# Optimization experiments

Measured on AMD Instinct MI355X. Metric: run time of the kernel, lower is better.

Reference implementation:

```python
import jax, jax.numpy as jnp
import numpy as np

MAX_WAVELENGTH = 10000.0
NUM_HEADS = 15
NUM_KV_HEADS = 5
HEAD_DIM = 64


def apply_rope(x, positions):
    """RoPE: x [B, L, H, D], positions [B, L] (int)."""
    d_half = x.shape[-1] // 2
    x = x.astype(jnp.float32)
    freq_exponents = (2.0 / x.shape[-1]) * jnp.arange(d_half, dtype=jnp.float32)
    timescale = MAX_WAVELENGTH ** freq_exponents  # [d_half]
    radians = positions[..., None].astype(jnp.float32) / timescale  # [B, L, d_half]
    radians = radians[..., None, :]  # [B, L, 1, d_half]
    sin, cos = jnp.sin(radians), jnp.cos(radians)
    x1, x2 = x[..., :d_half], x[..., d_half:]
    return jnp.concatenate([x1 * cos - x2 * sin, x2 * cos + x1 * sin], axis=-1)


def setup_inputs() -> dict:
    key = jax.random.key(0)
    k1, k2, k3, k4 = jax.random.split(key, 4)
    B, L = 2, 2048
    query_states = jax.random.normal(k1, (B, L, NUM_HEADS, HEAD_DIM), dtype=jnp.float32)
    key_states = jax.random.normal(k2, (B, L, NUM_KV_HEADS, HEAD_DIM), dtype=jnp.float32)
    value_states = jax.random.normal(k3, (B, L, NUM_KV_HEADS, HEAD_DIM), dtype=jnp.float32)
    positions = jnp.sort(jax.random.randint(k4, (B, L), 0, L, dtype=jnp.int32), axis=-1)
    # Causal (prefix-LM) boolean mask [B, L, L]
    attention_mask = jnp.broadcast_to(jnp.tril(jnp.ones((L, L), dtype=bool)), (B, L, L))
    return {
        "query_states": query_states,
        "key_states": key_states,
        "value_states": value_states,
        "positions": positions,
        "attention_mask": attention_mask,
    }


def reference(query_states, key_states, value_states, positions, attention_mask):
    B, L = query_states.shape[0], query_states.shape[1]
    groups = NUM_HEADS // NUM_KV_HEADS  # 3

    # RoPE on Q and K (eager, per original module)
    q = apply_rope(query_states, positions)  # [B, L, 15, 64] fp32
    k = apply_rope(key_states, positions)    # [B, L, 5, 64]  fp32

    # GQA expansion: [B, L, Kv, D] -> [B, L, Kv*groups, D]
    k = jnp.repeat(k, groups, axis=2)
    v = jnp.repeat(value_states, groups, axis=2).astype(jnp.float32)

    # Scores in fp32: [B, H, Lq, Lk]
    scores = jnp.einsum("bqhd,bkhd->bhqk", q, k) * (HEAD_DIM ** -0.5)
    big_neg = jnp.finfo(jnp.float32).min
    scores = jnp.where(attention_mask[:, None, :, :], scores, big_neg)
    probs = jax.nn.softmax(scores, axis=-1)

    out = jnp.einsum("bhqk,bkhd->bqhd", probs, v)  # [B, L, H, D]
    return out.reshape(B, L, NUM_HEADS * HEAD_DIM)  # [B, L, 960]
```

## Files before the change

kernel.cpp:

```cpp
#include <hip/hip_runtime.h>
#include <math.h>

#define NB 2
#define NL 2048
#define NHQ 15
#define NKV 5
#define HD 64
#define NT 32
#define GRP 3
#define PST 72
#define NG 16
#define SLOTF 2080

typedef __attribute__((ext_vector_type(8))) short short8;
typedef __attribute__((ext_vector_type(4))) float floatx4;

#define ROPE_C 0.28782313662425575f
#define QSCALE 0.18033688011116016f

__device__ __forceinline__ ushort f2bf(float x) {
    unsigned u = __builtin_bit_cast(unsigned, x);
    u = (u + 0x7FFFu + ((u >> 16) & 1u)) >> 16;
    return (ushort)u;
}
__device__ __forceinline__ unsigned pk2(float a, float b) {
    unsigned ua = __builtin_bit_cast(unsigned, a) + 0x8000u;
    unsigned ub = __builtin_bit_cast(unsigned, b) + 0x8000u;
    return __builtin_amdgcn_perm(ub, ua, 0x07060302u);
}
__device__ __forceinline__ void async16(ushort* lds, const ushort* g) {
    __builtin_amdgcn_global_load_lds(
        (const __attribute__((address_space(1))) unsigned int*)g,
        (__attribute__((address_space(3))) unsigned int*)lds, 16, 0, 0);
}

union U8  { short8 v; ushort u[8]; };
union F8  { float4 f4[2]; float f[8]; };

__global__ __launch_bounds__(256)
void prep_kv(const float* __restrict__ K, const float* __restrict__ V,
             const int* __restrict__ pos, ushort* __restrict__ Kr,
             ushort* __restrict__ Vr) {
    __shared__ float Vs[64][65];
    const int bid = blockIdx.x, t = threadIdx.x;
    if (bid < NB * NKV * NT) {
        int b = bid / (NKV * NT), rem = bid % (NKV * NT);
        int h = rem / NT, k0 = (rem % NT) * 64;
        int j = t >> 2, c0 = t & 3;
        int row = k0 + j;
        const float* src = K + ((size_t)((b * NL + row) * NKV + h)) * HD;
        int db = c0 * 8;
        F8 x1, x2;
        x1.f4[0] = *(const float4*)&src[db];
        x1.f4[1] = *(const float4*)&src[db + 4];
        x2.f4[0] = *(const float4*)&src[db + 32];
        x2.f4[1] = *(const float4*)&src[db + 36];
        float ps = (float)pos[b * NL + row];
        U8 lo, hi;
#pragma unroll
        for (int i = 0; i < 8; ++i) {
            float inv = __expf((float)(db + i) * -ROPE_C);
            float sn, cs; __sincosf(ps * inv, &sn, &cs);
            lo.u[i] = f2bf(x1.f[i] * cs - x2.f[i] * sn);
            hi.u[i] = f2bf(x2.f[i] * cs + x1.f[i] * sn);
        }
        ushort* dst = Kr + (size_t)bid * 4096;
        *(short8*)&dst[(j * 8 + (c0 ^ (j & 7))) * 8]       = lo.v;
        *(short8*)&dst[(j * 8 + ((c0 + 4) ^ (j & 7))) * 8] = hi.v;
    } else {
        int vb = bid - NB * NKV * NT;
        int b = vb / (NKV * NT), rem = vb % (NKV * NT);
        int h = rem / NT, k0 = (rem % NT) * 64;
#pragma unroll
        for (int it = 0; it < 4; ++it) {
            int e = t + it * 256;
            int j = e >> 4, d4 = (e & 15) * 4;
            *(float4*)&Vs[j][d4] =
                *(const float4*)&V[((size_t)((b * NL + k0 + j) * NKV + h)) * HD + d4];
        }
        __syncthreads();
        ushort* dst = Vr + (size_t)vb * 4096;
#pragma unroll
        for (int it = 0; it < 2; ++it) {
            int o = t + it * 256;
            int d = o >> 3, c = o & 7, j0 = c * 8;
            U8 r;
#pragma unroll
            for (int k = 0; k < 8; ++k) r.u[k] = f2bf(Vs[j0 + k][d]);
            *(short8*)&dst[(d * 8 + (c ^ (d & 7))) * 8] = r.v;
        }
    }
}

__global__ __launch_bounds__(256, 4)
void attn_partial(const float* __restrict__ Q, const ushort* __restrict__ Kr,
                  const ushort* __restrict__ Vr, const int* __restrict__ pos,
                  float* __restrict__ Pw, float* __restrict__ out,
                  int CH, int TOT) {
    __shared__ __align__(16) ushort Kb[4096];
    __shared__ __align__(16) ushort Vb[4096];
    __shared__ __align__(16) ushort Pb[4][2][16 * PST];

    const int t = threadIdx.x;
    const int w = t >> 6, lane = t & 63;
    const int l16 = lane & 15, quad = lane >> 4;
    const int h = blockIdx.y, b = blockIdx.z;
    const int kvh = h / GRP;
    const int fidx = TOT - 1 - (int)blockIdx.x;

    int g = 0, chunk = fidx;
    for (; g < NG; ++g) {
        int ncg = (2 * g + 2 + CH - 1) / CH;
        if (chunk < ncg) break;
        chunk -= ncg;
    }
    const int ntg = 2 * g + 2;
    const int nc  = (ntg + CH - 1) / CH;
    const int kb0 = chunk * CH;
    int kb1 = kb0 + CH; if (kb1 > ntg) kb1 = ntg;
    const int qi = 4 * g + w;
    const int ntw = (qi >> 1) + 1;
    const int r0 = qi * 32;

    short8 Qa[2][2];
#pragma unroll
    for (int rf = 0; rf < 2; ++rf) {
        int row = r0 + rf * 16 + l16;
        const float* src = Q + ((size_t)((b * NL + row) * NHQ + h)) * HD;
        int db = quad * 8;
        F8 x1, x2;
        x1.f4[0] = *(const float4*)&src[db];
        x1.f4[1] = *(const float4*)&src[db + 4];
        x2.f4[0] = *(const float4*)&src[db + 32];
        x2.f4[1] = *(const float4*)&src[db + 36];
        float ps = (float)pos[b * NL + row];
        union { short8 v; unsigned u[4]; } lo, hi;
#pragma unroll
        for (int i = 0; i < 8; i += 2) {
            float inv0 = __expf((float)(db + i) * -ROPE_C);
            float inv1 = __expf((float)(db + i + 1) * -ROPE_C);
            float sn0, cs0, sn1, cs1;
            __sincosf(ps * inv0, &sn0, &cs0);
            __sincosf(ps * inv1, &sn1, &cs1);
            float l0 = (x1.f[i] * cs0 - x2.f[i] * sn0) * QSCALE;
            float l1 = (x1.f[i + 1] * cs1 - x2.f[i + 1] * sn1) * QSCALE;
            float h0 = (x2.f[i] * cs0 + x1.f[i] * sn0) * QSCALE;
            float h1 = (x2.f[i + 1] * cs1 + x1.f[i + 1] * sn1) * QSCALE;
            lo.u[i >> 1] = pk2(l0, l1);
            hi.u[i >> 1] = pk2(h0, h1);
        }
        Qa[rf][0] = lo.v;
        Qa[rf][1] = hi.v;
    }

    floatx4 O[2][4];
    float lsum[2] = {0.f, 0.f};
#pragma unroll
    for (int rf = 0; rf < 2; ++rf)
#pragma unroll
        for (int d = 0; d < 4; ++d) O[rf][d] = (floatx4){0.f, 0.f, 0.f, 0.f};

    const ushort* Kt0 = Kr + (size_t)((b * NKV + kvh) * NT) * 4096;
    const ushort* Vt0 = Vr + (size_t)((b * NKV + kvh) * NT) * 4096;
    const int swz8[2] = { ((quad)     ^ (l16 & 7)) * 8,
                          ((quad + 4) ^ (l16 & 7)) * 8 };
    const int so = w * 1024;

    for (int kb = kb0; kb < kb1; ++kb) {
        {
            const ushort* Kt = Kt0 + (size_t)kb * 4096;
            const ushort* Vt = Vt0 + (size_t)kb * 4096;
            async16(&Kb[so],       Kt + so + lane * 8);
            async16(&Kb[so + 512], Kt + so + 512 + lane * 8);
            async16(&Vb[so],       Vt + so + lane * 8);
            async16(&Vb[so + 512], Vt + so + 512 + lane * 8);
        }
        __syncthreads();

        if (kb < ntw) {
            floatx4 S[2][4];
#pragma unroll
            for (int rf = 0; rf < 2; ++rf)
#pragma unroll
                for (int c = 0; c < 4; ++c) S[rf][c] = (floatx4){0.f, 0.f, 0.f, 0.f};
#pragma unroll
            for (int s = 0; s < 2; ++s)
#pragma unroll
                for (int c = 0; c < 4; ++c) {
                    short8 kfv = *(const short8*)&Kb[(c * 16 + l16) * 64 + swz8[s]];
                    S[0][c] = __builtin_amdgcn_mfma_f32_16x16x32_bf16(kfv, Qa[0][s], S[0][c], 0, 0, 0);
                    S[1][c] = __builtin_amdgcn_mfma_f32_16x16x32_bf16(kfv, Qa[1][s], S[1][c], 0, 0, 0);
                }

            if (kb == ntw - 1) {
#pragma unroll
                for (int rf = 0; rf < 2; ++rf) {
                    int qrow = r0 + rf * 16 + l16;
                    float acc = 0.f;
#pragma unroll
                    for (int c = 0; c < 4; ++c) {
                        float pv[4];
#pragma unroll
                        for (int r = 0; r < 4; ++r) {
                            int key = kb * 64 + c * 16 + quad * 4 + r;
                            float sv = S[rf][c][r];
                            if (key > qrow) sv = -1e30f;
                            pv[r] = exp2f(sv);
                            acc += pv[r];
                        }
                        *(uint2*)&Pb[w][rf][l16 * PST + c * 16 + quad * 4] =
                            make_uint2(pk2(pv[0], pv[1]), pk2(pv[2], pv[3]));
                    }
                    lsum[rf] += acc;
                }
            } else {
#pragma unroll
                for (int rf = 0; rf < 2; ++rf) {
                    float acc = 0.f;
#pragma unroll
                    for (int c = 0; c < 4; ++c) {
                        float pv[4];
#pragma unroll
                        for (int r = 0; r < 4; ++r) {
                            pv[r] = exp2f(S[rf][c][r]);
                            acc += pv[r];
                        }
                        *(uint2*)&Pb[w][rf][l16 * PST + c * 16 + quad * 4] =
                            make_uint2(pk2(pv[0], pv[1]), pk2(pv[2], pv[3]));
                    }
                    lsum[rf] += acc;
                }
            }

#pragma unroll
            for (int s = 0; s < 2; ++s) {
                short8 pf0 = *(const short8*)&Pb[w][0][l16 * PST + s * 32 + quad * 8];
                short8 pf1 = *(const short8*)&Pb[w][1][l16 * PST + s * 32 + quad * 8];
#pragma unroll
                for (int d = 0; d < 4; ++d) {
                    short8 vfv = *(const short8*)&Vb[(d * 16 + l16) * 64 + swz8[s]];
                    O[0][d] = __builtin_amdgcn_mfma_f32_16x16x32_bf16(vfv, pf0, O[0][d], 0, 0, 0);
                    O[1][d] = __builtin_amdgcn_mfma_f32_16x16x32_bf16(vfv, pf1, O[1][d], 0, 0, 0);
                }
            }
        }
        __syncthreads();
    }

    if (nc == 1) {
#pragma unroll
        for (int rf = 0; rf < 2; ++rf) {
            float ls = lsum[rf];
            ls += __shfl_xor(ls, 16, 64);
            ls += __shfl_xor(ls, 32, 64);
            float rinv = 1.0f / ls;
            int qrow = r0 + rf * 16 + l16;
            float* op = out + (size_t)(b * NL + qrow) * (NHQ * HD) + h * HD;
#pragma unroll
            for (int d = 0; d < 4; ++d) {
                float4 o = make_float4(O[rf][d][0] * rinv, O[rf][d][1] * rinv,
                                       O[rf][d][2] * rinv, O[rf][d][3] * rinv);
                *(float4*)&op[d * 16 + quad * 4] = o;
            }
        }
    } else {
        float* slot = Pw + (((size_t)(b * NHQ + h) * TOT + fidx) * 4 + w) * SLOTF;
#pragma unroll
        for (int rf = 0; rf < 2; ++rf) {
#pragma unroll
            for (int d = 0; d < 4; ++d) {
                float4 o = make_float4(O[rf][d][0], O[rf][d][1], O[rf][d][2], O[rf][d][3]);
                *(float4*)&slot[(rf * 16 + l16) * 64 + d * 16 + quad * 4] = o;
            }
            float ls = lsum[rf];
            ls += __shfl_xor(ls, 16, 64);
            ls += __shfl_xor(ls, 32, 64);
            if (quad == 0) slot[2048 + rf * 16 + l16] = ls;
        }
    }
}

__global__ __launch_bounds__(256)
void combine(const float* __restrict__ Pw, float* __restrict__ out,
             int CH, int TOT, int qi0) {
    __shared__ float ls[32];
    const int qi = qi0 + blockIdx.x;
    const int bh = blockIdx.y;
    const int b = bh / NHQ, h = bh % NHQ;
    const int g = qi >> 2, w = qi & 3;
    const int nch = (2 * g + 2 + CH - 1) / CH;
    int pfx = 0;
    for (int gg = 0; gg < g; ++gg) pfx += (2 * gg + 2 + CH - 1) / CH;
    const float* base = Pw + (((size_t)bh * TOT + pfx) * 4 + w) * SLOTF;

    const int t = threadIdx.x;
    const int rl = t >> 3, d0 = (t & 7) * 8;
    float a[8];
#pragma unroll
    for (int k = 0; k < 8; ++k) a[k] = 0.f;
    float lacc = 0.f;
    for (int c = 0; c < nch; ++c) {
        const float* pb = base + (size_t)c * 4 * SLOTF;
        float4 x0 = *(const float4*)&pb[rl * 64 + d0];
        float4 x1 = *(const float4*)&pb[rl * 64 + d0 + 4];
        a[0] += x0.x; a[1] += x0.y; a[2] += x0.z; a[3] += x0.w;
        a[4] += x1.x; a[5] += x1.y; a[6] += x1.z; a[7] += x1.w;
        if (t < 32) lacc += pb[2048 + t];
    }
    if (t < 32) ls[t] = lacc;
    __syncthreads();
    float rinv = 1.0f / ls[rl];
    float* op = out + (size_t)(b * NL + qi * 32 + rl) * (NHQ * HD) + h * HD + d0;
    *(float4*)&op[0] = make_float4(a[0] * rinv, a[1] * rinv, a[2] * rinv, a[3] * rinv);
    *(float4*)&op[4] = make_float4(a[4] * rinv, a[5] * rinv, a[6] * rinv, a[7] * rinv);
}

extern "C" void kernel_launch(void* const* d_in, const int* in_sizes, int n_in,
                              void* d_out, int out_size, void* d_ws, size_t ws_size,
                              hipStream_t stream) {
    const float* Q   = (const float*)d_in[0];
    const float* K   = (const float*)d_in[1];
    const float* V   = (const float*)d_in[2];
    const int*   pos = (const int*)d_in[3];
    ushort* Kr = (ushort*)d_ws;
    ushort* Vr = Kr + (size_t)NB * NKV * NT * 4096;
    float*  Pw = (float*)(Vr + (size_t)NB * NKV * NT * 4096);
    float*  out = (float*)d_out;
    const size_t prepBytes = (size_t)2 * NB * NKV * NT * 4096 * sizeof(ushort);

    int CH = 32, TOT = NG;
    const int ladder[3] = {4, 8, 16};
    for (int i = 0; i < 3; ++i) {
        int ch = ladder[i], tot = 0;
        for (int gq = 0; gq < NG; ++gq) tot += (2 * gq + 2 + ch - 1) / ch;
        size_t need = prepBytes + (size_t)NB * NHQ * tot * 4 * SLOTF * sizeof(float);
        if (need <= ws_size) { CH = ch; TOT = tot; break; }
    }

    prep_kv<<<2 * NB * NKV * NT, 256, 0, stream>>>(K, V, pos, Kr, Vr);
    dim3 grid(TOT, NHQ, NB);
    attn_partial<<<grid, 256, 0, stream>>>(Q, Kr, Vr, pos, Pw, out, CH, TOT);
    int qi0 = 2 * CH;
    if (qi0 < 64)
        combine<<<dim3(64 - qi0, NB * NHQ), 256, 0, stream>>>(Pw, out, CH, TOT, qi0);
}
```

Measured before the change: 150.8 us.

## Batch-load four K tiles into LDS and read V fragments from global

The attention loop now stages up to four K tiles at once into per-wave LDS buffers, so there is one barrier pair per four key blocks instead of per block. V fragments are read straight from global memory (L2) into registers rather than through LDS. The P buffer is shrunk to one row-fragment per wave, and waves stop at their own causal end. The fast hardware exp2 intrinsic replaces exp2f. The host chunk ladder now falls back to CH=16 instead of 32. Direct global V loads can expose memory latency that LDS staging used to hide.

```diff
diff --git a/kernel.cpp b/kernel.cpp
--- a/kernel.cpp
+++ b/kernel.cpp
@@ -97,9 +97,8 @@
                   const ushort* __restrict__ Vr, const int* __restrict__ pos,
                   float* __restrict__ Pw, float* __restrict__ out,
                   int CH, int TOT) {
-    __shared__ __align__(16) ushort Kb[4096];
-    __shared__ __align__(16) ushort Vb[4096];
-    __shared__ __align__(16) ushort Pb[4][2][16 * PST];
+    __shared__ __align__(16) ushort Kb[4][4096];
+    __shared__ __align__(16) ushort Pb[4][16 * PST];
 
     const int t = threadIdx.x;
     const int w = t >> 6, lane = t & 63;
@@ -121,6 +120,7 @@
     const int qi = 4 * g + w;
     const int ntw = (qi >> 1) + 1;
     const int r0 = qi * 32;
+    const int myEnd = (kb1 < ntw) ? kb1 : ntw;
 
     short8 Qa[2][2];
 #pragma unroll
@@ -164,20 +164,31 @@
     const ushort* Vt0 = Vr + (size_t)((b * NKV + kvh) * NT) * 4096;
     const int swz8[2] = { ((quad)     ^ (l16 & 7)) * 8,
                           ((quad + 4) ^ (l16 & 7)) * 8 };
-    const int so = w * 1024;
-
-    for (int kb = kb0; kb < kb1; ++kb) {
-        {
-            const ushort* Kt = Kt0 + (size_t)kb * 4096;
+
+    const int nt_c = kb1 - kb0;
+    for (int bi = 0; bi < nt_c; bi += 4) {
+        const int bcnt = (nt_c - bi < 4) ? (nt_c - bi) : 4;
+        if (bi) __syncthreads();
+        if (w < bcnt) {
+            const ushort* Kt = Kt0 + (size_t)(kb0 + bi + w) * 4096;
+#pragma unroll
+            for (int i = 0; i < 8; ++i)
+                async16(&Kb[w][i * 512], Kt + i * 512 + lane * 8);
+        }
+        __syncthreads();
+
+        for (int kbl = 0; kbl < bcnt; ++kbl) {
+            const int kb = kb0 + bi + kbl;
+            if (kb >= myEnd) break;
+
             const ushort* Vt = Vt0 + (size_t)kb * 4096;
-            async16(&Kb[so],       Kt + so + lane * 8);
-            async16(&Kb[so + 512], Kt + so + 512 + lane * 8);
-            async16(&Vb[so],       Vt + so + lane * 8);
-            async16(&Vb[so + 512], Vt + so + 512 + lane * 8);
-        }
-        __syncthreads();
-
-        if (kb < ntw) {
+            short8 vf[2][4];
+#pragma unroll
+            for (int s = 0; s < 2; ++s)
+#pragma unroll
+                for (int d = 0; d < 4; ++d)
+                    vf[s][d] = *(const short8*)(Vt + (d * 16 + l16) * 64 + swz8[s]);
+
             floatx4 S[2][4];
 #pragma unroll
             for (int rf = 0; rf < 2; ++rf)
@@ -187,16 +198,17 @@
             for (int s = 0; s < 2; ++s)
 #pragma unroll
                 for (int c = 0; c < 4; ++c) {
-                    short8 kfv = *(const short8*)&Kb[(c * 16 + l16) * 64 + swz8[s]];
+                    short8 kfv = *(const short8*)&Kb[kbl][(c * 16 + l16) * 64 + swz8[s]];
                     S[0][c] = __builtin_amdgcn_mfma_f32_16x16x32_bf16(kfv, Qa[0][s], S[0][c], 0, 0, 0);
                     S[1][c] = __builtin_amdgcn_mfma_f32_16x16x32_bf16(kfv, Qa[1][s], S[1][c], 0, 0, 0);
                 }
 
-            if (kb == ntw - 1) {
-#pragma unroll
-                for (int rf = 0; rf < 2; ++rf) {
+            const bool diag = (kb == ntw - 1);
+#pragma unroll
+            for (int rf = 0; rf < 2; ++rf) {
+                float acc = 0.f;
+                if (diag) {
                     int qrow = r0 + rf * 16 + l16;
-                    float acc = 0.f;
 #pragma unroll
                     for (int c = 0; c < 4; ++c) {
                         float pv[4];
@@ -205,46 +217,36 @@
                             int key = kb * 64 + c * 16 + quad * 4 + r;
                             float sv = S[rf][c][r];
                             if (key > qrow) sv = -1e30f;
-                            pv[r] = exp2f(sv);
+                            pv[r] = __builtin_amdgcn_exp2f(sv);
                             acc += pv[r];
                         }
-                        *(uint2*)&Pb[w][rf][l16 * PST + c * 16 + quad * 4] =
+                        *(uint2*)&Pb[w][l16 * PST + c * 16 + quad * 4] =
                             make_uint2(pk2(pv[0], pv[1]), pk2(pv[2], pv[3]));
                     }
-                    lsum[rf] += acc;
-                }
-            } else {
-#pragma unroll
-                for (int rf = 0; rf < 2; ++rf) {
-                    float acc = 0.f;
+                } else {
 #pragma unroll
                     for (int c = 0; c < 4; ++c) {
                         float pv[4];
 #pragma unroll
                         for (int r = 0; r < 4; ++r) {
-                            pv[r] = exp2f(S[rf][c][r]);
+                            pv[r] = __builtin_amdgcn_exp2f(S[rf][c][r]);
                             acc += pv[r];
                         }
-                        *(uint2*)&Pb[w][rf][l16 * PST + c * 16 + quad * 4] =
+                        *(uint2*)&Pb[w][l16 * PST + c * 16 + quad * 4] =
                             make_uint2(pk2(pv[0], pv[1]), pk2(pv[2], pv[3]));
                     }
-                    lsum[rf] += acc;
+                }
+                lsum[rf] += acc;
+
+                short8 pfA = *(const short8*)&Pb[w][l16 * PST + quad * 8];
+                short8 pfB = *(const short8*)&Pb[w][l16 * PST + 32 + quad * 8];
+#pragma unroll
+                for (int d = 0; d < 4; ++d) {
+                    O[rf][d] = __builtin_amdgcn_mfma_f32_16x16x32_bf16(vf[0][d], pfA, O[rf][d], 0, 0, 0);
+                    O[rf][d] = __builtin_amdgcn_mfma_f32_16x16x32_bf16(vf[1][d], pfB, O[rf][d], 0, 0, 0);
                 }
             }
-
-#pragma unroll
-            for (int s = 0; s < 2; ++s) {
-                short8 pf0 = *(const short8*)&Pb[w][0][l16 * PST + s * 32 + quad * 8];
-                short8 pf1 = *(const short8*)&Pb[w][1][l16 * PST + s * 32 + quad * 8];
-#pragma unroll
-                for (int d = 0; d < 4; ++d) {
-                    short8 vfv = *(const short8*)&Vb[(d * 16 + l16) * 64 + swz8[s]];
-                    O[0][d] = __builtin_amdgcn_mfma_f32_16x16x32_bf16(vfv, pf0, O[0][d], 0, 0, 0);
-                    O[1][d] = __builtin_amdgcn_mfma_f32_16x16x32_bf16(vfv, pf1, O[1][d], 0, 0, 0);
-                }
-            }
-        }
-        __syncthreads();
+        }
     }
 
     if (nc == 1) {
@@ -328,13 +330,20 @@
     float*  out = (float*)d_out;
     const size_t prepBytes = (size_t)2 * NB * NKV * NT * 4096 * sizeof(ushort);
 
-    int CH = 32, TOT = NG;
-    const int ladder[3] = {4, 8, 16};
-    for (int i = 0; i < 3; ++i) {
-        int ch = ladder[i], tot = 0;
-        for (int gq = 0; gq < NG; ++gq) tot += (2 * gq + 2 + ch - 1) / ch;
-        size_t need = prepBytes + (size_t)NB * NHQ * tot * 4 * SLOTF * sizeof(float);
-        if (need <= ws_size) { CH = ch; TOT = tot; break; }
+    int CH = 16, TOT = 0;
+    {
+        const int ladder[2] = {4, 8};
+        bool found = false;
+        for (int i = 0; i < 2 && !found; ++i) {
+            int ch = ladder[i], tot = 0;
+            for (int gq = 0; gq < NG; ++gq) tot += (2 * gq + 2 + ch - 1) / ch;
+            size_t need = prepBytes + (size_t)NB * NHQ * tot * 4 * SLOTF * sizeof(float);
+            if (need <= ws_size) { CH = ch; TOT = tot; found = true; }
+        }
+        if (!found) {
+            TOT = 0;
+            for (int gq = 0; gq < NG; ++gq) TOT += (2 * gq + 2 + CH - 1) / CH;
+        }
     }
 
     prep_kv<<<2 * NB * NKV * NT, 256, 0, stream>>>(K, V, pos, Kr, Vr);
```

After: 151.7 us. About the same (+0.6%).
